# Optimization experiments

Hardware: AMD Instinct MI355X
Metric: run time of the kernel (lower is better)

## Reference

```python
import jax, jax.numpy as jnp
import numpy as np

B, N, NPOINT, K = 8, 16384, 1024, 32
RADIUS = 0.2
SAMPLE_NUM = 10          # number of random subsets in get_robust_centroid
SEL = 7                  # round(10 * 0.7) centroids kept
SUBSET = int(round(K * 0.9))


def setup_inputs() -> dict:
    key = jax.random.key(0)
    xyz = jax.random.normal(key, (B, N, 3), dtype=jnp.float32)
    return {"xyz": xyz}


def _batched_gather(points, idx):
    # points: [B, N, C], idx: [B, ...] -> [B, ..., C]
    return jax.vmap(lambda p, i: p[i])(points, idx)


def _fps(xyz, npoint):
    # Sequential farthest point sampling -> indices [B, npoint]
    Bb, Nn, _ = xyz.shape
    init = (jnp.full((Bb, Nn), 1e10, xyz.dtype), jnp.zeros((Bb,), jnp.int32))

    def body(carry, _):
        distance, farthest = carry
        centroid = _batched_gather(xyz, farthest)            # [B, 3]
        dist = jnp.sum((xyz - centroid[:, None, :]) ** 2, -1)  # [B, N]
        distance = jnp.minimum(distance, dist)
        new_far = jnp.argmax(distance, axis=-1).astype(jnp.int32)
        return (distance, new_far), farthest

    _, idx = jax.lax.scan(body, init, None, length=npoint)
    return idx.T  # [B, npoint]


def _knn_idx(xyz, centers, k):
    # squared-distance matrix [B, S, N], then k smallest (torch.cdist + topk)
    d2 = (jnp.sum(centers ** 2, -1)[:, :, None]
          + jnp.sum(xyz ** 2, -1)[:, None, :]
          - 2.0 * jnp.einsum('bsc,bnc->bsn', centers, xyz))
    _, idx = jax.lax.top_k(-d2, k)
    return idx  # [B, S, k]


def _robust_centroid(grouped):
    # grouped: [B, S, K, 3] -> robust centroid [B, S, 3]
    key = jax.random.key(42)
    cents = []
    for i in range(SAMPLE_NUM):
        perm = jax.random.permutation(jax.random.fold_in(key, i), K)
        cents.append(jnp.mean(grouped[:, :, perm[:SUBSET], :], axis=2))
    cl = jnp.stack(cents, axis=2)                             # [B, S, 10, 3]
    sq = jnp.sum(cl ** 2, -1, keepdims=True)                  # [B, S, 10, 1]
    pd = sq + jnp.swapaxes(sq, -1, -2) - 2.0 * jnp.einsum('bsik,bsjk->bsij', cl, cl)
    pd_sum = jnp.sum(pd, -1)                                  # [B, S, 10]
    _, order = jax.lax.top_k(-pd_sum, SAMPLE_NUM)             # ascending by dist-sum
    sel = order[..., :SEL]                                    # [B, S, 7]
    sel_b = jnp.broadcast_to(sel[..., None], sel.shape + (3,))
    csel = jnp.take_along_axis(cl, sel_b, axis=2)             # [B, S, 7, 3]
    return jnp.mean(csel, axis=2)


def _global_feature(new_xyz, radius, grouped_xyz):
    centroid_xyz = _robust_centroid(grouped_xyz)              # [B, S, 3]
    ref_norm = jnp.linalg.norm(new_xyz, axis=-1, keepdims=True)
    ref_unit = new_xyz / (ref_norm + 1e-4)
    inter_xyz = radius * ref_unit + new_xyz
    crv = new_xyz - centroid_xyz
    crd = jnp.linalg.norm(crv, axis=-1, keepdims=True)
    civ = inter_xyz - centroid_xyz
    cid = jnp.linalg.norm(civ, axis=-1, keepdims=True)
    dot = jnp.sum(crv * civ, -1, keepdims=True)
    ang_rci = dot / (crd * cid + 1e-6)
    irv = new_xyz - inter_xyz
    icv = centroid_xyz - inter_xyz
    dot2 = jnp.sum(irv * icv, -1, keepdims=True)
    ang_ric = dot2 / (radius * cid + 1e-6)
    return jnp.concatenate([ref_norm, crd, cid, ang_rci, ang_ric], axis=-1)  # [B, S, 5]


def reference(xyz):
    cent_idx = _fps(xyz, NPOINT)                   # [B, S]
    centers = _batched_gather(xyz, cent_idx)       # [B, S, 3]
    nn_idx = _knn_idx(xyz, centers, K)             # [B, S, K]
    grouped = _batched_gather(xyz, nn_idx)         # [B, S, K, 3]
    return _global_feature(centers, RADIUS, grouped)
```

## Files before the change

kernel.cpp:

```cpp
#include <hip/hip_runtime.h>
#include <stdint.h>
#include <algorithm>

#define BATCH 8
#define NPTS 16384
#define NPOINT 1024
#define KNN 32
#define SAMPLE_NUM 10
#define SELN 7
#define SUBSET 29
#define RADIUS 0.2f
#define CAP 2048

struct PermTab { unsigned char p[SAMPLE_NUM][SUBSET]; };

static inline uint32_t rotl32h(uint32_t x, int d) { return (x << d) | (x >> (32 - d)); }

static void tf2x32(uint32_t k0, uint32_t k1, uint32_t c0, uint32_t c1,
                   uint32_t& o0, uint32_t& o1) {
    const uint32_t ks[3] = { k0, k1, k0 ^ k1 ^ 0x1BD11BDAu };
    uint32_t x0 = c0 + ks[0];
    uint32_t x1 = c1 + ks[1];
    static const int R[8] = {13, 15, 26, 6, 17, 29, 16, 24};
    for (int s = 0; s < 5; ++s) {
        const int* r = R + (s % 2) * 4;
        for (int j = 0; j < 4; ++j) {
            x0 += x1;
            x1 = rotl32h(x1, r[j]);
            x1 ^= x0;
        }
        x0 += ks[(s + 1) % 3];
        x1 += ks[(s + 2) % 3] + (uint32_t)(s + 1);
    }
    o0 = x0; o1 = x1;
}

static PermTab build_tab() {
    PermTab t;
    for (int i = 0; i < SAMPLE_NUM; ++i) {
        uint32_t f0, f1;
        tf2x32(0u, 42u, 0u, (uint32_t)i, f0, f1);
        uint32_t s0, s1;
        tf2x32(f0, f1, 0u, 1u, s0, s1);
        uint32_t bits[32];
        for (int j = 0; j < 32; ++j) {
            uint32_t o0, o1;
            tf2x32(s0, s1, 0u, (uint32_t)j, o0, o1);
            bits[j] = o0 ^ o1;
        }
        int perm[32];
        for (int j = 0; j < 32; ++j) perm[j] = j;
        std::stable_sort(perm, perm + 32, [&](int x, int y) {
            return bits[x] < bits[y];
        });
        for (int q = 0; q < SUBSET; ++q) t.p[i][q] = (unsigned char)perm[q];
    }
    return t;
}

#define REP32(M) M(0) M(1) M(2) M(3) M(4) M(5) M(6) M(7) \
                 M(8) M(9) M(10) M(11) M(12) M(13) M(14) M(15) \
                 M(16) M(17) M(18) M(19) M(20) M(21) M(22) M(23) \
                 M(24) M(25) M(26) M(27) M(28) M(29) M(30) M(31)

__global__ __launch_bounds__(512, 2) void fps_kernel(const float* __restrict__ xyz,
                                                     float* __restrict__ centers,
                                                     float* __restrict__ sx) {
#pragma clang fp contract(off)
    const int b = blockIdx.x;
    const int tid = threadIdx.x;
    const int wv = tid >> 6;
    const int lane = tid & 63;

    __shared__ unsigned long long skey[2][8];

    const float* base = xyz + (size_t)b * NPTS * 3;

#define P_DECL(i) float px##i, py##i, pz##i, dd##i;
    REP32(P_DECL)
#undef P_DECL

#define P_LOAD(i) { \
        const int p = (i) * 512 + tid; \
        px##i = base[p * 3 + 0]; \
        py##i = base[p * 3 + 1]; \
        pz##i = base[p * 3 + 2]; \
        dd##i = 1e10f; \
        sx[(size_t)b * NPTS + p] = (px##i * px##i + py##i * py##i) + pz##i * pz##i; }
    REP32(P_LOAD)
#undef P_LOAD

#define P_PIN(i) asm volatile("" : "+v"(px##i), "+v"(py##i), "+v"(pz##i));
    REP32(P_PIN)
#undef P_PIN

    float cx = base[0], cy = base[1], cz = base[2];
    if (tid == 0) {
        float* dst = centers + (size_t)b * NPOINT * 3;
        dst[0] = cx; dst[1] = cy; dst[2] = cz;
    }
    __syncthreads();

    for (int t = 1; t < NPOINT; ++t) {
        const int par = t & 1;
        float bv = -1.0f;
        int bi = 0;
#define P_SCAN(i) { \
        const float dx = px##i - cx; \
        const float dy = py##i - cy; \
        const float dz = pz##i - cz; \
        const float d = dx * dx + dy * dy + dz * dz; \
        const float nd = fminf(dd##i, d); \
        dd##i = nd; \
        if (nd > bv) { bv = nd; bi = (i); } }
        REP32(P_SCAN)
#undef P_SCAN

        const unsigned bp = ((unsigned)bi << 9) | (unsigned)tid;
        unsigned long long key =
            ((unsigned long long)__float_as_uint(bv) << 32) |
            (unsigned long long)(0xFFFFFFFFu - bp);
#pragma unroll
        for (int m = 32; m >= 1; m >>= 1) {
            unsigned long long o = __shfl_xor(key, m, 64);
            key = (o > key) ? o : key;
        }
        if (lane == 0) skey[par][wv] = key;
        __syncthreads();

        unsigned long long kk = skey[par][0];
#pragma unroll
        for (int q = 1; q < 8; ++q) {
            const unsigned long long kq = skey[par][q];
            kk = (kq > kk) ? kq : kk;
        }

        const int p = (int)(0xFFFFFFFFu - (unsigned)(kk & 0xFFFFFFFFull));
        const int ps = __builtin_amdgcn_readfirstlane(p);
        const float* sp = base + (size_t)ps * 3;
        cx = sp[0]; cy = sp[1]; cz = sp[2];

        if (tid == 0) {
            float* dst = centers + ((size_t)b * NPOINT + t) * 3;
            dst[0] = cx; dst[1] = cy; dst[2] = cz;
        }
    }
}

__global__ __launch_bounds__(256) void knn_kernel(const float* __restrict__ xyz,
                                                  const float* __restrict__ centers,
                                                  const float* __restrict__ sx,
                                                  float* __restrict__ grouped) {
    const int bs = blockIdx.x;
    const int b = bs >> 10;
    const int tid = threadIdx.x;

    __shared__ unsigned hist[2048];
    __shared__ unsigned ckey[CAP];
    __shared__ int cidx[CAP];
    __shared__ int cnt;
    __shared__ int bstar;

    const float cx = centers[(size_t)bs * 3 + 0];
    const float cy = centers[(size_t)bs * 3 + 1];
    const float cz = centers[(size_t)bs * 3 + 2];
    const float sc = __fadd_rn(__fadd_rn(__fmul_rn(cx, cx), __fmul_rn(cy, cy)),
                               __fmul_rn(cz, cz));

    for (int q = tid; q < 2048; q += 256) hist[q] = 0;
    if (tid == 0) cnt = 0;
    __syncthreads();

    const float* base = xyz + (size_t)b * NPTS * 3;
    const float* sxb = sx + (size_t)b * NPTS;

    for (int j = tid; j < NPTS; j += 256) {
        float xx = base[j * 3 + 0], xy = base[j * 3 + 1], xz = base[j * 3 + 2];
        float dot = __fadd_rn(__fadd_rn(__fmul_rn(cx, xx), __fmul_rn(cy, xy)),
                              __fmul_rn(cz, xz));
        float d2 = __fsub_rn(__fadd_rn(sc, sxb[j]), __fmul_rn(2.0f, dot));
        unsigned u = __float_as_uint(d2);
        unsigned key = u ^ ((u & 0x80000000u) ? 0xFFFFFFFFu : 0x80000000u);
        atomicAdd(&hist[key >> 21], 1u);
    }
    __syncthreads();

    if (tid < 64) {
        unsigned sum = 0;
#pragma unroll
        for (int q = 0; q < 32; ++q) sum += hist[tid * 32 + q];
        unsigned incl = sum;
        for (int d = 1; d < 64; d <<= 1) {
            unsigned o = __shfl_up(incl, d, 64);
            if (tid >= d) incl += o;
        }
        unsigned long long m = __ballot(incl >= 32u);
        int L = __ffsll(m) - 1;
        if (tid == L) {
            unsigned cum = incl - sum;
            int bb = L * 32 + 31;
            for (int q = 0; q < 32; ++q) {
                cum += hist[L * 32 + q];
                if (cum >= 32u) { bb = L * 32 + q; break; }
            }
            bstar = bb;
        }
    }
    __syncthreads();

    const int bst = bstar;
    for (int j = tid; j < NPTS; j += 256) {
        float xx = base[j * 3 + 0], xy = base[j * 3 + 1], xz = base[j * 3 + 2];
        float dot = __fadd_rn(__fadd_rn(__fmul_rn(cx, xx), __fmul_rn(cy, xy)),
                              __fmul_rn(cz, xz));
        float d2 = __fsub_rn(__fadd_rn(sc, sxb[j]), __fmul_rn(2.0f, dot));
        unsigned u = __float_as_uint(d2);
        unsigned key = u ^ ((u & 0x80000000u) ? 0xFFFFFFFFu : 0x80000000u);
        if ((int)(key >> 21) <= bst) {
            int pos = atomicAdd(&cnt, 1);
            if (pos < CAP) { ckey[pos] = key; cidx[pos] = j; }
        }
    }
    __syncthreads();

    const int L2 = min(cnt, CAP);
    for (int c = tid; c < L2; c += 256) {
        const unsigned k = ckey[c];
        const int id = cidx[c];
        int rank = 0;
        for (int m2 = 0; m2 < L2; ++m2) {
            const unsigned km = ckey[m2];
            rank += (km < k || (km == k && cidx[m2] < id)) ? 1 : 0;
        }
        if (rank < KNN) {
            float* dst = grouped + ((size_t)bs * KNN + rank) * 3;
            dst[0] = base[id * 3 + 0];
            dst[1] = base[id * 3 + 1];
            dst[2] = base[id * 3 + 2];
        }
    }
}

__global__ __launch_bounds__(256) void feat_kernel(const float* __restrict__ centers,
                                                   const float* __restrict__ grouped,
                                                   float* __restrict__ out,
                                                   PermTab tab) {
    const int bs = blockIdx.x * 256 + threadIdx.x;
    if (bs >= BATCH * NPOINT) return;

    const float* g = grouped + (size_t)bs * KNN * 3;

    float clx[SAMPLE_NUM], cly[SAMPLE_NUM], clz[SAMPLE_NUM];
    for (int i = 0; i < SAMPLE_NUM; ++i) {
        float sxm = 0.f, sym = 0.f, szm = 0.f;
        for (int j = 0; j < SUBSET; ++j) {
            const int p = tab.p[i][j];
            sxm = __fadd_rn(sxm, g[p * 3 + 0]);
            sym = __fadd_rn(sym, g[p * 3 + 1]);
            szm = __fadd_rn(szm, g[p * 3 + 2]);
        }
        clx[i] = __fdiv_rn(sxm, 29.0f);
        cly[i] = __fdiv_rn(sym, 29.0f);
        clz[i] = __fdiv_rn(szm, 29.0f);
    }

    float sq[SAMPLE_NUM];
#pragma unroll
    for (int i = 0; i < SAMPLE_NUM; ++i)
        sq[i] = __fadd_rn(__fadd_rn(__fmul_rn(clx[i], clx[i]), __fmul_rn(cly[i], cly[i])),
                          __fmul_rn(clz[i], clz[i]));

    float ps[SAMPLE_NUM];
#pragma unroll
    for (int i = 0; i < SAMPLE_NUM; ++i) {
        float pd[SAMPLE_NUM];
#pragma unroll
        for (int j = 0; j < SAMPLE_NUM; ++j) {
            float dot = __fadd_rn(__fadd_rn(__fmul_rn(clx[i], clx[j]), __fmul_rn(cly[i], cly[j])),
                                  __fmul_rn(clz[i], clz[j]));
            pd[j] = __fsub_rn(__fadd_rn(sq[i], sq[j]), __fmul_rn(2.0f, dot));
        }
        float res = __fadd_rn(__fadd_rn(__fadd_rn(pd[0], pd[1]), __fadd_rn(pd[2], pd[3])),
                              __fadd_rn(__fadd_rn(pd[4], pd[5]), __fadd_rn(pd[6], pd[7])));
        res = __fadd_rn(res, pd[8]);
        res = __fadd_rn(res, pd[9]);
        ps[i] = res;
    }

    int rnk[SAMPLE_NUM];
#pragma unroll
    for (int j = 0; j < SAMPLE_NUM; ++j) {
        int r = 0;
#pragma unroll
        for (int m = 0; m < SAMPLE_NUM; ++m)
            r += (ps[m] < ps[j] || (ps[m] == ps[j] && m < j)) ? 1 : 0;
        rnk[j] = r;
    }

    float csx = 0.f, csy = 0.f, csz = 0.f;
    for (int r = 0; r < SELN; ++r) {
#pragma unroll
        for (int j = 0; j < SAMPLE_NUM; ++j) {
            if (rnk[j] == r) {
                csx = __fadd_rn(csx, clx[j]);
                csy = __fadd_rn(csy, cly[j]);
                csz = __fadd_rn(csz, clz[j]);
            }
        }
    }
    const float ccx = __fdiv_rn(csx, 7.0f);
    const float ccy = __fdiv_rn(csy, 7.0f);
    const float ccz = __fdiv_rn(csz, 7.0f);

    const float nx = centers[(size_t)bs * 3 + 0];
    const float ny = centers[(size_t)bs * 3 + 1];
    const float nz = centers[(size_t)bs * 3 + 2];

    const float ref_norm = __fsqrt_rn(__fadd_rn(
        __fadd_rn(__fmul_rn(nx, nx), __fmul_rn(ny, ny)), __fmul_rn(nz, nz)));
    const float den = __fadd_rn(ref_norm, 1e-4f);
    const float ux = __fdiv_rn(nx, den), uy = __fdiv_rn(ny, den), uz = __fdiv_rn(nz, den);
    const float ix = __fadd_rn(__fmul_rn(RADIUS, ux), nx);
    const float iy = __fadd_rn(__fmul_rn(RADIUS, uy), ny);
    const float iz = __fadd_rn(__fmul_rn(RADIUS, uz), nz);

    const float crvx = __fsub_rn(nx, ccx), crvy = __fsub_rn(ny, ccy), crvz = __fsub_rn(nz, ccz);
    const float crd = __fsqrt_rn(__fadd_rn(
        __fadd_rn(__fmul_rn(crvx, crvx), __fmul_rn(crvy, crvy)), __fmul_rn(crvz, crvz)));
    const float civx = __fsub_rn(ix, ccx), civy = __fsub_rn(iy, ccy), civz = __fsub_rn(iz, ccz);
    const float cid = __fsqrt_rn(__fadd_rn(
        __fadd_rn(__fmul_rn(civx, civx), __fmul_rn(civy, civy)), __fmul_rn(civz, civz)));
    const float dot = __fadd_rn(__fadd_rn(__fmul_rn(crvx, civx), __fmul_rn(crvy, civy)),
                                __fmul_rn(crvz, civz));
    const float ang_rci = __fdiv_rn(dot, __fadd_rn(__fmul_rn(crd, cid), 1e-6f));

    const float irvx = __fsub_rn(nx, ix), irvy = __fsub_rn(ny, iy), irvz = __fsub_rn(nz, iz);
    const float icvx = __fsub_rn(ccx, ix), icvy = __fsub_rn(ccy, iy), icvz = __fsub_rn(ccz, iz);
    const float dot2 = __fadd_rn(__fadd_rn(__fmul_rn(irvx, icvx), __fmul_rn(irvy, icvy)),
                                 __fmul_rn(irvz, icvz));
    const float ang_ric = __fdiv_rn(dot2, __fadd_rn(__fmul_rn(RADIUS, cid), 1e-6f));

    float* o = out + (size_t)bs * 5;
    o[0] = ref_norm;
    o[1] = crd;
    o[2] = cid;
    o[3] = ang_rci;
    o[4] = ang_ric;
}

extern "C" void kernel_launch(void* const* d_in, const int* in_sizes, int n_in,
                              void* d_out, int out_size, void* d_ws, size_t ws_size,
                              hipStream_t stream) {
    const float* xyz = (const float*)d_in[0];
    float* out = (float*)d_out;

    float* centers = (float*)d_ws;
    float* sx = centers + (size_t)BATCH * NPOINT * 3;
    float* grouped = sx + (size_t)BATCH * NPTS;

    static PermTab tab = build_tab();

    fps_kernel<<<BATCH, 512, 0, stream>>>(xyz, centers, sx);
    knn_kernel<<<BATCH * NPOINT, 256, 0, stream>>>(xyz, centers, sx, grouped);
    feat_kernel<<<(BATCH * NPOINT + 255) / 256, 256, 0, stream>>>(centers, grouped, out, tab);
}
```

Baseline: 2.050 ms.

## Widen FPS blocks to 1024 threads and use DPP row reductions for argmax

The farthest-point-sampling kernel now runs 1024 threads per batch instead of 512, so each thread holds 16 points in registers instead of 32 and the per-iteration serial scan is shorter. The wave-level argmax reduction swaps shuffle-xor steps for DPP row_shr and row_bcast steps, with lane 63 holding the result. The cross-wave reduce over 16 waves also uses DPP across lanes instead of a serial loop over shared memory. The cost is more waves joining each barrier, and the key ordering relies on DPP bound_ctrl behaviour and a lane-15 readlane being correct.

```diff
diff --git a/kernel.cpp b/kernel.cpp
--- a/kernel.cpp
+++ b/kernel.cpp
@@ -58,40 +58,49 @@
     return t;
 }
 
-#define REP32(M) M(0) M(1) M(2) M(3) M(4) M(5) M(6) M(7) \
-                 M(8) M(9) M(10) M(11) M(12) M(13) M(14) M(15) \
-                 M(16) M(17) M(18) M(19) M(20) M(21) M(22) M(23) \
-                 M(24) M(25) M(26) M(27) M(28) M(29) M(30) M(31)
-
-__global__ __launch_bounds__(512, 2) void fps_kernel(const float* __restrict__ xyz,
-                                                     float* __restrict__ centers,
-                                                     float* __restrict__ sx) {
+#define REP16(M) M(0) M(1) M(2) M(3) M(4) M(5) M(6) M(7) \
+                 M(8) M(9) M(10) M(11) M(12) M(13) M(14) M(15)
+
+#define DPP_MAX_STEP(var, ctrl) { \
+        const unsigned lo_ = (unsigned)(var); \
+        const unsigned hi_ = (unsigned)((var) >> 32); \
+        const unsigned olo_ = (unsigned)__builtin_amdgcn_update_dpp( \
+            (int)lo_, (int)lo_, (ctrl), 0xf, 0xf, false); \
+        const unsigned ohi_ = (unsigned)__builtin_amdgcn_update_dpp( \
+            (int)hi_, (int)hi_, (ctrl), 0xf, 0xf, false); \
+        const unsigned long long o_ = \
+            ((unsigned long long)ohi_ << 32) | (unsigned long long)olo_; \
+        (var) = (o_ > (var)) ? o_ : (var); }
+
+__global__ __launch_bounds__(1024, 4) void fps_kernel(const float* __restrict__ xyz,
+                                                      float* __restrict__ centers,
+                                                      float* __restrict__ sx) {
 #pragma clang fp contract(off)
     const int b = blockIdx.x;
     const int tid = threadIdx.x;
     const int wv = tid >> 6;
     const int lane = tid & 63;
 
-    __shared__ unsigned long long skey[2][8];
+    __shared__ unsigned long long skey[2][16];
 
     const float* base = xyz + (size_t)b * NPTS * 3;
 
 #define P_DECL(i) float px##i, py##i, pz##i, dd##i;
-    REP32(P_DECL)
+    REP16(P_DECL)
 #undef P_DECL
 
 #define P_LOAD(i) { \
-        const int p = (i) * 512 + tid; \
+        const int p = (i) * 1024 + tid; \
         px##i = base[p * 3 + 0]; \
         py##i = base[p * 3 + 1]; \
         pz##i = base[p * 3 + 2]; \
         dd##i = 1e10f; \
         sx[(size_t)b * NPTS + p] = (px##i * px##i + py##i * py##i) + pz##i * pz##i; }
-    REP32(P_LOAD)
+    REP16(P_LOAD)
 #undef P_LOAD
 
 #define P_PIN(i) asm volatile("" : "+v"(px##i), "+v"(py##i), "+v"(pz##i));
-    REP32(P_PIN)
+    REP16(P_PIN)
 #undef P_PIN
 
     float cx = base[0], cy = base[1], cz = base[2];
@@ -113,30 +122,32 @@
         const float nd = fminf(dd##i, d); \
         dd##i = nd; \
         if (nd > bv) { bv = nd; bi = (i); } }
-        REP32(P_SCAN)
+        REP16(P_SCAN)
 #undef P_SCAN
 
-        const unsigned bp = ((unsigned)bi << 9) | (unsigned)tid;
+        const unsigned bp = ((unsigned)bi << 10) | (unsigned)tid;
         unsigned long long key =
             ((unsigned long long)__float_as_uint(bv) << 32) |
             (unsigned long long)(0xFFFFFFFFu - bp);
-#pragma unroll
-        for (int m = 32; m >= 1; m >>= 1) {
-            unsigned long long o = __shfl_xor(key, m, 64);
-            key = (o > key) ? o : key;
-        }
-        if (lane == 0) skey[par][wv] = key;
+
+        DPP_MAX_STEP(key, 0x111)
+        DPP_MAX_STEP(key, 0x112)
+        DPP_MAX_STEP(key, 0x114)
+        DPP_MAX_STEP(key, 0x118)
+        DPP_MAX_STEP(key, 0x142)
+        DPP_MAX_STEP(key, 0x143)
+        if (lane == 63) skey[par][wv] = key;
         __syncthreads();
 
-        unsigned long long kk = skey[par][0];
-#pragma unroll
-        for (int q = 1; q < 8; ++q) {
-            const unsigned long long kq = skey[par][q];
-            kk = (kq > kk) ? kq : kk;
-        }
-
-        const int p = (int)(0xFFFFFFFFu - (unsigned)(kk & 0xFFFFFFFFull));
-        const int ps = __builtin_amdgcn_readfirstlane(p);
+        unsigned long long kk = skey[par][lane & 15];
+        DPP_MAX_STEP(kk, 0x111)
+        DPP_MAX_STEP(kk, 0x112)
+        DPP_MAX_STEP(kk, 0x114)
+        DPP_MAX_STEP(kk, 0x118)
+
+        const unsigned klo = (unsigned)__builtin_amdgcn_readlane((int)(unsigned)kk, 15);
+        const int ps = __builtin_amdgcn_readfirstlane(
+            (int)(0xFFFFFFFFu - klo));
         const float* sp = base + (size_t)ps * 3;
         cx = sp[0]; cy = sp[1]; cz = sp[2];
 
@@ -360,7 +371,7 @@
 
     static PermTab tab = build_tab();
 
-    fps_kernel<<<BATCH, 512, 0, stream>>>(xyz, centers, sx);
+    fps_kernel<<<BATCH, 1024, 0, stream>>>(xyz, centers, sx);
     knn_kernel<<<BATCH * NPOINT, 256, 0, stream>>>(xyz, centers, sx, grouped);
     feat_kernel<<<(BATCH * NPOINT + 255) / 256, 256, 0, stream>>>(centers, grouped, out, tab);
 }
```

Result: faster. 1.964 ms (-4.2%).

## Restructure FPS kernel: 1024 threads, LDS-staged xy, packed math, DPP argmax reduction

Applied to the files above, without the earlier changes.

Doubles the FPS block to 1024 threads, so each thread holds 16 points instead of 32. The x/y coordinates are staged in LDS as pairs and only z and running distances stay in registers. Distance updates use two-wide float vectors. The 64-bit shuffle argmax is replaced by a two-pass 32-bit DPP reduction: a max over values, then a max over the inverted index among ties, followed by a 16-wave cross-wave reduction. This aims to shorten the serial per-iteration latency of the 1023-step FPS loop, at the cost of LDS reads in the inner loop and more waves joining each barrier.

```diff
diff --git a/kernel.cpp b/kernel.cpp
--- a/kernel.cpp
+++ b/kernel.cpp
@@ -11,6 +11,9 @@
 #define SUBSET 29
 #define RADIUS 0.2f
 #define CAP 2048
+
+typedef float f32x2 __attribute__((ext_vector_type(2)));
+typedef float f32x4 __attribute__((ext_vector_type(4)));
 
 struct PermTab { unsigned char p[SAMPLE_NUM][SUBSET]; };
 
@@ -58,40 +61,56 @@
     return t;
 }
 
-#define REP32(M) M(0) M(1) M(2) M(3) M(4) M(5) M(6) M(7) \
-                 M(8) M(9) M(10) M(11) M(12) M(13) M(14) M(15) \
-                 M(16) M(17) M(18) M(19) M(20) M(21) M(22) M(23) \
-                 M(24) M(25) M(26) M(27) M(28) M(29) M(30) M(31)
-
-__global__ __launch_bounds__(512, 2) void fps_kernel(const float* __restrict__ xyz,
-                                                     float* __restrict__ centers,
-                                                     float* __restrict__ sx) {
+#define REP8(M) M(0) M(1) M(2) M(3) M(4) M(5) M(6) M(7)
+
+#define DPP_FMAX_STEP(v, ctrl) { \
+        const int t_ = __builtin_amdgcn_update_dpp( \
+            __float_as_int(v), __float_as_int(v), (ctrl), 0xf, 0xf, false); \
+        (v) = fmaxf((v), __int_as_float(t_)); }
+
+#define DPP_UMAX_STEP(v, ctrl) { \
+        const unsigned t_ = (unsigned)__builtin_amdgcn_update_dpp( \
+            (int)(v), (int)(v), (ctrl), 0xf, 0xf, false); \
+        (v) = (t_ > (v)) ? t_ : (v); }
+
+__global__ __launch_bounds__(1024) void fps_kernel(const float* __restrict__ xyz,
+                                                   float* __restrict__ centers,
+                                                   float* __restrict__ sqout) {
 #pragma clang fp contract(off)
     const int b = blockIdx.x;
     const int tid = threadIdx.x;
     const int wv = tid >> 6;
     const int lane = tid & 63;
 
-    __shared__ unsigned long long skey[2][8];
+    __shared__ f32x4 sPair[NPTS / 2];
+    __shared__ unsigned skhi[2][16];
+    __shared__ unsigned sklo[2][16];
 
     const float* base = xyz + (size_t)b * NPTS * 3;
 
-#define P_DECL(i) float px##i, py##i, pz##i, dd##i;
-    REP32(P_DECL)
+#define P_DECL(j) f32x2 pz2##j, dd2##j;
+    REP8(P_DECL)
 #undef P_DECL
 
-#define P_LOAD(i) { \
-        const int p = (i) * 512 + tid; \
-        px##i = base[p * 3 + 0]; \
-        py##i = base[p * 3 + 1]; \
-        pz##i = base[p * 3 + 2]; \
-        dd##i = 1e10f; \
-        sx[(size_t)b * NPTS + p] = (px##i * px##i + py##i * py##i) + pz##i * pz##i; }
-    REP32(P_LOAD)
+#define P_LOAD(j) { \
+        const int q = (j) * 1024 + tid; \
+        const f32x2 a = *(const f32x2*)&base[6 * q]; \
+        const f32x2 b2 = *(const f32x2*)&base[6 * q + 2]; \
+        const f32x2 c = *(const f32x2*)&base[6 * q + 4]; \
+        const f32x2 px2 = (f32x2){a.x, b2.y}; \
+        const f32x2 py2 = (f32x2){a.y, c.x}; \
+        pz2##j = (f32x2){b2.x, c.y}; \
+        dd2##j = (f32x2){1e10f, 1e10f}; \
+        sPair[q] = (f32x4){px2.x, px2.y, py2.x, py2.y}; \
+        const f32x2 xx = px2 * px2, yy = py2 * py2, zz = pz2##j * pz2##j; \
+        const f32x2 s1 = xx + yy; \
+        const f32x2 dsq = s1 + zz; \
+        *(f32x2*)&sqout[(size_t)b * NPTS + 2 * q] = dsq; }
+    REP8(P_LOAD)
 #undef P_LOAD
 
-#define P_PIN(i) asm volatile("" : "+v"(px##i), "+v"(py##i), "+v"(pz##i));
-    REP32(P_PIN)
+#define P_PIN(j) asm volatile("" : "+v"(pz2##j));
+    REP8(P_PIN)
 #undef P_PIN
 
     float cx = base[0], cy = base[1], cz = base[2];
@@ -103,42 +122,74 @@
 
     for (int t = 1; t < NPOINT; ++t) {
         const int par = t & 1;
+        const f32x2 ccx2 = (f32x2){cx, cx};
+        const f32x2 ccy2 = (f32x2){cy, cy};
+        const f32x2 ccz2 = (f32x2){cz, cz};
         float bv = -1.0f;
-        int bi = 0;
-#define P_SCAN(i) { \
-        const float dx = px##i - cx; \
-        const float dy = py##i - cy; \
-        const float dz = pz##i - cz; \
-        const float d = dx * dx + dy * dy + dz * dz; \
-        const float nd = fminf(dd##i, d); \
-        dd##i = nd; \
-        if (nd > bv) { bv = nd; bi = (i); } }
-        REP32(P_SCAN)
+        unsigned bidx = 0;
+#define P_SCAN(j) { \
+        const f32x4 vv = sPair[(j) * 1024 + tid]; \
+        const f32x2 dx = (f32x2){vv.x, vv.y} - ccx2; \
+        const f32x2 dy = (f32x2){vv.z, vv.w} - ccy2; \
+        const f32x2 dz = pz2##j - ccz2; \
+        const f32x2 xx = dx * dx; \
+        const f32x2 yy = dy * dy; \
+        const f32x2 zz = dz * dz; \
+        const f32x2 ss = xx + yy; \
+        const f32x2 d = ss + zz; \
+        const float nd0 = fminf(dd2##j.x, d.x); \
+        const float nd1 = fminf(dd2##j.y, d.y); \
+        dd2##j.x = nd0; dd2##j.y = nd1; \
+        if (nd0 > bv) { bv = nd0; bidx = (j) * 2; } \
+        if (nd1 > bv) { bv = nd1; bidx = (j) * 2 + 1; } }
+        REP8(P_SCAN)
 #undef P_SCAN
 
-        const unsigned bp = ((unsigned)bi << 9) | (unsigned)tid;
-        unsigned long long key =
-            ((unsigned long long)__float_as_uint(bv) << 32) |
-            (unsigned long long)(0xFFFFFFFFu - bp);
-#pragma unroll
-        for (int m = 32; m >= 1; m >>= 1) {
-            unsigned long long o = __shfl_xor(key, m, 64);
-            key = (o > key) ? o : key;
-        }
-        if (lane == 0) skey[par][wv] = key;
+        float r = bv;
+        DPP_FMAX_STEP(r, 0x111)
+        DPP_FMAX_STEP(r, 0x112)
+        DPP_FMAX_STEP(r, 0x114)
+        DPP_FMAX_STEP(r, 0x118)
+        DPP_FMAX_STEP(r, 0x142)
+        DPP_FMAX_STEP(r, 0x143)
+        const float wmax = __int_as_float(
+            __builtin_amdgcn_readlane(__float_as_int(r), 63));
+
+        const unsigned p = ((bidx >> 1) << 11) + ((unsigned)tid << 1) + (bidx & 1);
+        unsigned uk = (bv == wmax) ? ~p : 0u;
+        DPP_UMAX_STEP(uk, 0x111)
+        DPP_UMAX_STEP(uk, 0x112)
+        DPP_UMAX_STEP(uk, 0x114)
+        DPP_UMAX_STEP(uk, 0x118)
+        DPP_UMAX_STEP(uk, 0x142)
+        DPP_UMAX_STEP(uk, 0x143)
+
+        if (lane == 63) {
+            skhi[par][wv] = __float_as_uint(r);
+            sklo[par][wv] = uk;
+        }
         __syncthreads();
 
-        unsigned long long kk = skey[par][0];
-#pragma unroll
-        for (int q = 1; q < 8; ++q) {
-            const unsigned long long kq = skey[par][q];
-            kk = (kq > kk) ? kq : kk;
-        }
-
-        const int p = (int)(0xFFFFFFFFu - (unsigned)(kk & 0xFFFFFFFFull));
-        const int ps = __builtin_amdgcn_readfirstlane(p);
-        const float* sp = base + (size_t)ps * 3;
-        cx = sp[0]; cy = sp[1]; cz = sp[2];
+        const unsigned myhi = skhi[par][lane & 15];
+        const unsigned mylo = sklo[par][lane & 15];
+        unsigned h2 = myhi;
+        DPP_UMAX_STEP(h2, 0x111)
+        DPP_UMAX_STEP(h2, 0x112)
+        DPP_UMAX_STEP(h2, 0x114)
+        DPP_UMAX_STEP(h2, 0x118)
+        const unsigned shi = (unsigned)__builtin_amdgcn_readlane((int)h2, 15);
+        unsigned c2 = (myhi == shi) ? mylo : 0u;
+        DPP_UMAX_STEP(c2, 0x111)
+        DPP_UMAX_STEP(c2, 0x112)
+        DPP_UMAX_STEP(c2, 0x114)
+        DPP_UMAX_STEP(c2, 0x118)
+        const unsigned slo = (unsigned)__builtin_amdgcn_readlane((int)c2, 15);
+        const int ps = (int)(~slo);
+
+        const float* wrow = (const float*)&sPair[ps >> 1];
+        cx = wrow[ps & 1];
+        cy = wrow[2 + (ps & 1)];
+        cz = base[(size_t)ps * 3 + 2];
 
         if (tid == 0) {
             float* dst = centers + ((size_t)b * NPOINT + t) * 3;
@@ -360,7 +411,7 @@
 
     static PermTab tab = build_tab();
 
-    fps_kernel<<<BATCH, 512, 0, stream>>>(xyz, centers, sx);
+    fps_kernel<<<BATCH, 1024, 0, stream>>>(xyz, centers, sx);
     knn_kernel<<<BATCH * NPOINT, 256, 0, stream>>>(xyz, centers, sx, grouped);
     feat_kernel<<<(BATCH * NPOINT + 255) / 256, 256, 0, stream>>>(centers, grouped, out, tab);
 }
```

After: 1.992 ms. -2.8%, faster.
